# Performance work log

Hardware: AMD Instinct MI355X
Metric: run time of the kernel (lower is better)

## Reference

```python
import jax, jax.numpy as jnp
import numpy as np

B, S, F_IN, F_OUT = 8, 128, 768, 768
NUM_REL = 41           # num_dependencies + 1
NUM_LAYER = 2
N_HEAD, HID = 8, 96    # hidden_dim = embed_dim // n_head
EMB = 768


def setup_inputs() -> dict:
    key = jax.random.key(0)
    ks = jax.random.split(key, 14)
    s = 1.0 / np.sqrt(F_IN)
    inp = {
        "x": jax.random.normal(ks[0], (B, S, F_IN), dtype=jnp.float32),
        "adj": jax.random.uniform(ks[1], (B, NUM_REL, S, S), dtype=jnp.float32),
        "q": jax.random.normal(ks[2], (B, EMB), dtype=jnp.float32),
        # R-GCN params (stacked over layers)
        "w_rgcn": jax.random.uniform(ks[3], (NUM_LAYER, NUM_REL, F_IN, F_OUT), minval=-s, maxval=s),
        "score_w": jax.random.uniform(ks[4], (NUM_LAYER, F_OUT), minval=-s, maxval=s),
        "score_b": jax.random.uniform(ks[5], (NUM_LAYER,), minval=-s, maxval=s),
        # Attention params (stored as [in, out] for x @ W)
        "wk": jax.random.uniform(ks[6], (EMB, N_HEAD * HID), minval=-s, maxval=s),
        "bk": jnp.zeros((N_HEAD * HID,), jnp.float32),
        "wq": jax.random.uniform(ks[7], (EMB, N_HEAD * HID), minval=-s, maxval=s),
        "bq": jnp.zeros((N_HEAD * HID,), jnp.float32),
        "wbil": jax.random.uniform(ks[8], (HID, HID), minval=-1.0 / np.sqrt(HID), maxval=1.0 / np.sqrt(HID)),
        "wproj": jax.random.uniform(ks[9], (N_HEAD * HID, EMB), minval=-s, maxval=s),
        "bproj": jnp.zeros((EMB,), jnp.float32),
    }
    return inp


def _rgcn_layer(h, adj, w, sw, sb):
    # h: [B,S,I]; adj: [B,R,S,S]; w: [R,I,O]
    hidden = jnp.einsum("bsi,rio->brso", h, w)            # per-relation transform
    denom = jnp.sum(adj, axis=3, keepdims=True)           # [B,R,S,1]
    intm = jnp.einsum("brsk,brko->brso", adj, hidden)     # relation-wise aggregation
    div = intm / jnp.where(denom == 0, jnp.ones_like(denom), denom)
    logits = jnp.einsum("brso,o->brs", div, sw) + sb      # score Linear(out->1)
    r_coeffs = jax.nn.softmax(logits, axis=1)             # softmax over relations
    out = jnp.einsum("brso,brs->bso", div, r_coeffs)
    return jax.nn.relu(out)


def _attention(k, q, wk, bk, wq, bq, wbil, wproj, bproj):
    # k: [B,S,E]; q: [B,E] -> [B,1,E]
    q3 = q[:, None, :]
    kx = (k @ wk + bk).reshape(B, S, N_HEAD, HID)
    qx = (q3 @ wq + bq).reshape(B, 1, N_HEAD, HID)
    qw = jnp.einsum("bqhd,de->bqhe", qx, wbil)            # bi_linear score
    score = jnp.einsum("bqhe,bkhe->bhqk", qw, kx)
    attn = jax.nn.softmax(score, axis=-1)
    o = jnp.einsum("bhqk,bkhd->bqhd", attn, kx).reshape(B, 1, N_HEAD * HID)
    return o @ wproj + bproj                              # [B,1,EMB]


def reference(x, adj, q, w_rgcn, score_w, score_b, wk, bk, wq, bq, wbil, wproj, bproj):
    h = x
    for l in range(NUM_LAYER):
        h = _rgcn_layer(h, adj, w_rgcn[l], score_w[l], score_b[l])
    return _attention(h, q, wk, bk, wq, bq, wbil, wproj, bproj)
```

## Files before the change

kernel.cpp:

```cpp
#include <hip/hip_runtime.h>
#include <stdint.h>

#define B_ 8
#define S_ 128
#define R_ 41
#define F_ 768
#define NH_ 8
#define HID_ 96
#define BS_ (B_*S_)
#define SM_SCALE 256.0f
#define NG_ 21
#define NWV_ (R_*12)

typedef _Float16 f16;
typedef _Float16 f16x8 __attribute__((ext_vector_type(8)));
typedef _Float16 f16x4 __attribute__((ext_vector_type(4)));
typedef _Float16 f16x2 __attribute__((ext_vector_type(2)));
typedef float f32x4 __attribute__((ext_vector_type(4)));
typedef float f32x2 __attribute__((ext_vector_type(2)));

#define GLD16(gp, lp) __builtin_amdgcn_global_load_lds((const __attribute__((address_space(1))) uint32_t*)(gp), (__attribute__((address_space(3))) uint32_t*)(lp), 16, 0, 0)

__device__ __forceinline__ float wredsum(float v){
  #pragma unroll
  for (int o=32;o;o>>=1) v += __shfl_down(v,o,64);
  return v;
}

__global__ __launch_bounds__(256) void kPrep(const float* __restrict__ w_rgcn, const float* __restrict__ score_w,
                                             const float* __restrict__ wk, const float* __restrict__ x,
                                             const float* __restrict__ qin, const float* __restrict__ wq,
                                             const float* __restrict__ bq, const float* __restrict__ wbil,
                                             f16* __restrict__ wT0, f16* __restrict__ wT1,
                                             float* __restrict__ v0, float* __restrict__ v1,
                                             f16* __restrict__ wkT, f16* __restrict__ h16T,
                                             float* __restrict__ qwb) {
  __shared__ float sbuf[64*68];
  int bid = blockIdx.x;
  int tid = threadIdx.x;
  if (bid < 2*NWV_) {
    int l = (bid >= NWV_);
    int sub = bid - l*NWV_;
    const float* w = w_rgcn + (size_t)l*R_*F_*F_;
    const float* sw = score_w + l*F_;
    f16* wT = l ? wT1 : wT0;
    float* v = l ? v1 : v0;
    int it = sub % 12, r = sub / 12;
    int ri = tid >> 2, c = tid & 3;
    float vacc = 0.f;
    for (int ot = 0; ot < 12; ++ot) {
      const float* src = w + ((size_t)r*F_ + (it*64 + ri))*F_ + ot*64 + c*16;
      const float* swp = sw + ot*64 + c*16;
      __syncthreads();
      #pragma unroll
      for (int j=0;j<4;j++){
        f32x4 v4 = *(const f32x4*)(src + j*4);
        f32x4 s4 = *(const f32x4*)(swp + j*4);
        vacc += v4.x*s4.x + v4.y*s4.y + v4.z*s4.z + v4.w*s4.w;
        *(f32x4*)&sbuf[ri*68 + c*16 + j*4] = v4;
      }
      __syncthreads();
      int ro = tid >> 2;
      f16 outv[16];
      #pragma unroll
      for (int j=0;j<16;j++) outv[j] = (f16)sbuf[(c*16+j)*68 + ro];
      f16* dst = wT + ((size_t)r*F_ + (ot*64+ro))*F_ + it*64 + c*16;
      *(f16x8*)dst = *(f16x8*)&outv[0];
      *(f16x8*)(dst+8) = *(f16x8*)&outv[8];
    }
    vacc += __shfl_down(vacc, 1, 64);
    vacc += __shfl_down(vacc, 2, 64);
    if (c == 0) v[(size_t)r*F_ + it*64 + ri] = vacc;
  } else if (bid < 2*NWV_ + 144) {
    int sub = bid - 2*NWV_;
    int ot = sub % 12; int it = sub / 12;
    int ri = tid >> 2, c = tid & 3;
    const float* src = wk + (size_t)(it*64 + ri)*F_ + ot*64 + c*16;
    #pragma unroll
    for (int j=0;j<4;j++){
      f32x4 v4 = *(const f32x4*)(src + j*4);
      *(f32x4*)&sbuf[ri*68 + c*16 + j*4] = v4;
    }
    __syncthreads();
    int ro = tid >> 2;
    f16 outv[16];
    #pragma unroll
    for (int j=0;j<16;j++) outv[j] = (f16)sbuf[(c*16+j)*68 + ro];
    f16* dst = wkT + (size_t)(ot*64+ro)*F_ + it*64 + c*16;
    *(f16x8*)dst = *(f16x8*)&outv[0];
    *(f16x8*)(dst+8) = *(f16x8*)&outv[8];
  } else if (bid < 2*NWV_ + 144 + 192) {
    int sub = bid - (2*NWV_ + 144);
    int st = sub & 1; int ft = (sub>>1) % 12; int b = sub / 24;
    f16* t = (f16*)sbuf;
    int sl = tid>>2, c = tid&3;
    const float* src = x + ((size_t)b*S_ + st*64 + sl)*F_ + ft*64 + c*16;
    f16 tmp[16];
    #pragma unroll
    for (int j=0;j<16;j++) tmp[j] = (f16)src[j];
    *(f16x8*)&t[sl*72 + c*16]     = *(f16x8*)&tmp[0];
    *(f16x8*)&t[sl*72 + c*16 + 8] = *(f16x8*)&tmp[8];
    __syncthreads();
    int fl = tid>>2;
    f16 outv[16];
    #pragma unroll
    for (int j=0;j<16;j++) outv[j] = t[(c*16+j)*72 + fl];
    f16* dst = h16T + ((size_t)b*F_ + ft*64 + fl)*S_ + st*64 + c*16;
    *(f16x8*)dst = *(f16x8*)&outv[0];
    *(f16x8*)(dst+8) = *(f16x8*)&outv[8];
  } else {
    int sub = bid - (2*NWV_ + 144 + 192);
    int h = sub & 7, b = sub >> 3;
    float* q_s = sbuf;
    float* qx_s = sbuf + 768;
    for (int j=tid; j<F_; j+=256) q_s[j] = qin[(size_t)b*F_ + j];
    __syncthreads();
    if (tid < 192){
      int e = tid>>1, half = tid&1;
      const float* wp = wq + (size_t)(half*384)*F_ + h*HID_ + e;
      const float* qp = q_s + half*384;
      float a0=0.f,a1=0.f,a2=0.f,a3=0.f;
      for (int i=0;i<384;i+=4){
        a0 += qp[i]  *wp[(size_t)i*F_];
        a1 += qp[i+1]*wp[(size_t)(i+1)*F_];
        a2 += qp[i+2]*wp[(size_t)(i+2)*F_];
        a3 += qp[i+3]*wp[(size_t)(i+3)*F_];
      }
      float s2 = a0+a1+a2+a3;
      s2 += __shfl_xor(s2,1,64);
      if (half==0) qx_s[e] = s2 + bq[h*HID_+e];
    }
    __syncthreads();
    if (tid < HID_){
      float a0=0.f,a1=0.f,a2=0.f,a3=0.f;
      for (int d=0;d<HID_;d+=4){
        a0 += qx_s[d]  *wbil[(size_t)d*HID_+tid];
        a1 += qx_s[d+1]*wbil[(size_t)(d+1)*HID_+tid];
        a2 += qx_s[d+2]*wbil[(size_t)(d+2)*HID_+tid];
        a3 += qx_s[d+3]*wbil[(size_t)(d+3)*HID_+tid];
      }
      qwb[(size_t)b*F_ + h*HID_ + tid] = a0+a1+a2+a3;
    }
  }
}

__global__ __launch_bounds__(256) void kUL(const float* __restrict__ h, const float* __restrict__ v,
                    const float* __restrict__ adj, const float* __restrict__ sb_all, int l,
                    float* __restrict__ dinv, float* __restrict__ lg) {
  int bid = blockIdx.x;
  int r = bid % R_, b = bid / R_;
  __shared__ float v_s[F_];
  __shared__ float u_s[S_];
  int tid = threadIdx.x;
  #pragma unroll
  for (int j=0;j<3;j++) v_s[tid + j*256] = v[(size_t)r*F_ + tid + j*256];
  __syncthreads();
  int wid = tid>>6, lane = tid&63;
  for (int kl=0; kl<32; ++kl){
    int k = wid*32 + kl;
    const float* hr = h + ((size_t)b*S_ + k)*F_ + lane*12;
    const float* vp = &v_s[lane*12];
    float acc=0.f;
    #pragma unroll
    for (int j=0;j<3;j++){
      f32x4 a = *(const f32x4*)(hr+j*4);
      f32x4 c4 = *(const f32x4*)(vp+j*4);
      acc += a.x*c4.x+a.y*c4.y+a.z*c4.z+a.w*c4.w;
    }
    acc = wredsum(acc);
    if (lane==0) u_s[k] = acc;
  }
  __syncthreads();
  int s = tid>>1, half = tid&1;
  const float* arow = adj + ((size_t)bid*S_ + s)*S_ + half*64;
  const float* up = &u_s[half*64];
  float ssum=0.f, sdot=0.f;
  #pragma unroll
  for (int j=0;j<16;j++){
    f32x4 a = *(const f32x4*)(arow + j*4);
    ssum += a.x+a.y+a.z+a.w;
    sdot += a.x*up[j*4] + a.y*up[j*4+1] + a.z*up[j*4+2] + a.w*up[j*4+3];
  }
  ssum += __shfl_xor(ssum,1,64);
  sdot += __shfl_xor(sdot,1,64);
  if (half==0){
    float dv = (ssum==0.0f)?1.0f:(1.0f/ssum);
    dinv[(size_t)bid*S_ + s] = dv;
    lg[(size_t)bid*S_ + s] = sdot*dv + sb_all[l];
  }
}

__global__ __launch_bounds__(64) void kSM16(const float* __restrict__ lg, const float* __restrict__ dinv,
                     const float* __restrict__ adj, f16* __restrict__ M) {
  int bid = blockIdx.x;
  int b = bid >> 7, s = bid & 127;
  int lane = threadIdx.x;
  __shared__ float coef[R_];
  float x = (lane < R_) ? lg[((size_t)b*R_ + lane)*S_ + s] : -1e30f;
  float m = x;
  #pragma unroll
  for (int o=32;o;o>>=1) m = fmaxf(m, __shfl_xor(m,o,64));
  float e = (lane < R_) ? expf(x - m) : 0.f;
  float sum = e;
  #pragma unroll
  for (int o=32;o;o>>=1) sum += __shfl_xor(sum,o,64);
  if (lane < R_) coef[lane] = e/sum * SM_SCALE * dinv[((size_t)b*R_ + lane)*S_ + s];
  __syncthreads();
  for (int r=0;r<R_;r++){
    float cc = coef[r];
    size_t base = (((size_t)(b*R_+r))*S_ + s)*S_ + lane*2;
    f32x2 a2 = *(const f32x2*)(adj + base);
    f16x2 o2; o2[0]=(f16)(a2.x*cc); o2[1]=(f16)(a2.y*cc);
    *(f16x2*)(M + base) = o2;
  }
}

__global__ __launch_bounds__(256) void kGgemm(const f16* __restrict__ M, const f16* __restrict__ hT, f16* __restrict__ G) {
  __shared__ f16 lds[2*16384];
  f16* lsA = lds;
  f16* lsB = lds + 16384;
  int bid = blockIdx.x;
  int nt = bid % 6; int r = (bid/6) % R_; int b = bid/(6*R_);
  int tid = threadIdx.x, wid = tid>>6, lane = tid&63;
  const f16* Ab = M + (size_t)(b*R_ + r)*(S_*S_);
  const f16* Bb = hT + ((size_t)b*F_ + nt*128)*S_;
  #pragma unroll
  for (int j=0;j<8;j++){
    int qd = wid*8 + j;
    GLD16(Ab + qd*512 + lane*8, lsA + qd*512);
    GLD16(Bb + qd*512 + lane*8, lsB + qd*512);
  }
  __syncthreads();
  f32x4 acc[4][4] = {};
  int wr = wid>>1, wc = wid&1;
  int lr = lane&15, kk0 = (lane>>4)*8;
  #pragma unroll
  for (int ks=0;ks<4;ks++){
    int kk = ks*32 + kk0;
    f16x8 av[4], bv[4];
    #pragma unroll
    for (int i=0;i<4;i++) av[i] = *(const f16x8*)&lsA[(wr*64+i*16+lr)*128 + kk];
    #pragma unroll
    for (int i=0;i<4;i++) bv[i] = *(const f16x8*)&lsB[(wc*64+i*16+lr)*128 + kk];
    #pragma unroll
    for (int mi=0;mi<4;mi++)
      #pragma unroll
      for (int ni=0;ni<4;ni++)
        acc[mi][ni] = __builtin_amdgcn_mfma_f32_16x16x32_f16(av[mi],bv[ni],acc[mi][ni],0,0,0);
  }
  __syncthreads();
  #pragma unroll
  for (int mi=0;mi<4;mi++)
    #pragma unroll
    for (int ni=0;ni<4;ni++){
      int row = wr*64 + mi*16 + (lane>>4)*4;
      int col = wc*64 + ni*16 + lr;
      #pragma unroll
      for (int i=0;i<4;i++)
        lds[(row+i)*136 + col] = (f16)acc[mi][ni][i];
    }
  __syncthreads();
  int row = tid>>1, seg = tid&1;
  f16* dst = G + ((size_t)(b*R_ + r)*S_ + row)*F_ + nt*128 + seg*64;
  const f16* sl = lds + row*136 + seg*64;
  #pragma unroll
  for (int j=0;j<8;j++) *(f16x8*)(dst + j*8) = *(const f16x8*)(sl + j*8);
}

__global__ __launch_bounds__(512,2) void kOutGemm(const f16* __restrict__ G, const f16* __restrict__ WT, float* __restrict__ Cp) {
  __shared__ f16 ls[2][2][256*64];
  int bid = blockIdx.x;
  int t12 = bid % 12, g = bid / 12;
  int nt = t12 % 3, mt = t12 / 3;
  int r0 = (g<20)? 2*g : 40;
  int nr = (g<20)? 2 : 1;
  int tid = threadIdx.x, wid = tid>>6, lane = tid&63;
  size_t abase[4], bbase[4];
  #pragma unroll
  for (int j=0;j<4;j++){
    int chunk = wid*4 + j;
    int arow = mt*256 + chunk*8 + (lane>>3);
    int b = arow >> 7, s = arow & 127;
    abase[j] = ((size_t)b*R_*S_ + s)*(size_t)F_ + (lane&7)*8;
    int orow = nt*256 + chunk*8 + (lane>>3);
    bbase[j] = (size_t)orow*F_ + (lane&7)*8;
  }
  f32x4 acc[8][4] = {};
  int wr = wid>>2, wc = wid&3;
  int lr = lane&15, kk0 = (lane>>4)*8;
  int nsteps = nr*12;
  auto STAGE = [&](int bf, int step){
    int r = r0 + step/12, it = step%12;
    const f16* Ar = G  + (size_t)r*S_*F_;
    const f16* Br = WT + (size_t)r*F_*F_;
    #pragma unroll
    for (int j=0;j<4;j++){
      int chunk = wid*4 + j;
      GLD16(Ar + abase[j] + it*64, &ls[bf][0][chunk*512]);
      GLD16(Br + bbase[j] + it*64, &ls[bf][1][chunk*512]);
    }
  };
  STAGE(0, 0);
  __syncthreads();
  int cur = 0;
  for (int step=0; step<nsteps; ++step){
    if (step+1 < nsteps) STAGE(cur^1, step+1);
    __builtin_amdgcn_s_setprio(1);
    #pragma unroll
    for (int ks=0;ks<2;ks++){
      int kk = ks*32 + kk0;
      f16x8 av[8], bv[4];
      #pragma unroll
      for (int i=0;i<8;i++) av[i] = *(const f16x8*)&ls[cur][0][(wr*128+i*16+lr)*64 + kk];
      #pragma unroll
      for (int i=0;i<4;i++) bv[i] = *(const f16x8*)&ls[cur][1][(wc*64+i*16+lr)*64 + kk];
      #pragma unroll
      for (int mi=0;mi<8;mi++)
        #pragma unroll
        for (int ni=0;ni<4;ni++)
          acc[mi][ni] = __builtin_amdgcn_mfma_f32_16x16x32_f16(av[mi],bv[ni],acc[mi][ni],0,0,0);
    }
    __builtin_amdgcn_s_setprio(0);
    __syncthreads();
    cur ^= 1;
  }
  #pragma unroll
  for (int mi=0;mi<8;mi++)
    #pragma unroll
    for (int ni=0;ni<4;ni++){
      int row = mt*256 + wr*128 + mi*16 + (lane>>4)*4;
      int col = nt*256 + wc*64 + ni*16 + lr;
      #pragma unroll
      for (int i=0;i<4;i++)
        Cp[((size_t)g*BS_ + row + i)*F_ + col] = acc[mi][ni][i];
    }
}

__global__ __launch_bounds__(256) void kReduceT(const float* __restrict__ Cp, float* __restrict__ h32,
                                                f16* __restrict__ h16o, f16* __restrict__ hT) {
  int bid = blockIdx.x;
  int st = bid & 1; int ft = (bid>>1) % 12; int b = bid / 24;
  __shared__ f16 t[64*72];
  int tid = threadIdx.x;
  int sl = tid>>2, c = tid&3;
  size_t base = ((size_t)(b*S_ + st*64 + sl))*F_ + ft*64 + c*16;
  const float inv = 1.0f/SM_SCALE;
  f16 tmp[16];
  #pragma unroll
  for (int q=0;q<4;q++){
    f32x4 s4 = {};
    #pragma unroll
    for (int g=0; g<NG_; g++){
      f32x4 v4 = *(const f32x4*)(Cp + (size_t)g*BS_*F_ + base + q*4);
      s4.x += v4.x; s4.y += v4.y; s4.z += v4.z; s4.w += v4.w;
    }
    f32x4 rr;
    rr.x = fmaxf(s4.x*inv, 0.f); rr.y = fmaxf(s4.y*inv, 0.f);
    rr.z = fmaxf(s4.z*inv, 0.f); rr.w = fmaxf(s4.w*inv, 0.f);
    *(f32x4*)(h32 + base + q*4) = rr;
    tmp[q*4+0]=(f16)rr.x; tmp[q*4+1]=(f16)rr.y; tmp[q*4+2]=(f16)rr.z; tmp[q*4+3]=(f16)rr.w;
  }
  *(f16x8*)&t[sl*72 + c*16]     = *(f16x8*)&tmp[0];
  *(f16x8*)&t[sl*72 + c*16 + 8] = *(f16x8*)&tmp[8];
  *(f16x8*)(h16o + base)     = *(f16x8*)&tmp[0];
  *(f16x8*)(h16o + base + 8) = *(f16x8*)&tmp[8];
  __syncthreads();
  int fl = tid>>2;
  f16 outv[16];
  #pragma unroll
  for (int j=0;j<16;j++) outv[j] = t[(c*16+j)*72 + fl];
  f16* dst = hT + ((size_t)b*F_ + ft*64 + fl)*S_ + st*64 + c*16;
  *(f16x8*)dst = *(f16x8*)&outv[0];
  *(f16x8*)(dst+8) = *(f16x8*)&outv[8];
}

__global__ __launch_bounds__(256) void kKx(const f16* __restrict__ A, const f16* __restrict__ BT,
                    const float* __restrict__ bias, float* __restrict__ C) {
  __shared__ f16 ls[2][2][128*64];
  int bid = blockIdx.x;
  int nt = bid % 6, mt = bid / 6;
  int tid = threadIdx.x, wid = tid>>6, lane = tid&63;
  size_t abase[4], bbase[4];
  #pragma unroll
  for (int j=0;j<4;j++){
    int qd = wid*4 + j;
    int row = mt*128 + qd*8 + (lane>>3);
    abase[j] = (size_t)row*F_ + (lane&7)*8;
    int o = nt*128 + qd*8 + (lane>>3);
    bbase[j] = (size_t)o*F_ + (lane&7)*8;
  }
  f32x4 acc[4][4] = {};
  int wr = wid>>1, wc = wid&1;
  int lr = lane&15, kk0 = (lane>>4)*8;
  auto STAGE = [&](int bf, int it){
    #pragma unroll
    for (int j=0;j<4;j++){
      int qd = wid*4+j;
      GLD16(A + abase[j] + it*64, &ls[bf][0][qd*512]);
      GLD16(BT + bbase[j] + it*64, &ls[bf][1][qd*512]);
    }
  };
  STAGE(0, 0);
  __syncthreads();
  int cur = 0;
  for (int it=0; it<12; ++it){
    if (it+1 < 12) STAGE(cur^1, it+1);
    #pragma unroll
    for (int ks=0;ks<2;ks++){
      int kk = ks*32 + kk0;
      f16x8 av[4], bv[4];
      #pragma unroll
      for (int i=0;i<4;i++) av[i] = *(const f16x8*)&ls[cur][0][(wr*64+i*16+lr)*64 + kk];
      #pragma unroll
      for (int i=0;i<4;i++) bv[i] = *(const f16x8*)&ls[cur][1][(wc*64+i*16+lr)*64 + kk];
      #pragma unroll
      for (int mi=0;mi<4;mi++)
        #pragma unroll
        for (int ni=0;ni<4;ni++)
          acc[mi][ni] = __builtin_amdgcn_mfma_f32_16x16x32_f16(av[mi],bv[ni],acc[mi][ni],0,0,0);
    }
    __syncthreads();
    cur ^= 1;
  }
  #pragma unroll
  for (int mi=0;mi<4;mi++)
    #pragma unroll
    for (int ni=0;ni<4;ni++){
      int row = mt*128 + wr*64 + mi*16 + (lane>>4)*4;
      int col = nt*128 + wc*64 + ni*16 + lr;
      float bb = bias[col];
      #pragma unroll
      for (int i=0;i<4;i++)
        C[(size_t)(row+i)*F_ + col] = acc[mi][ni][i] + bb;
    }
}

__global__ __launch_bounds__(256) void kAttnCore(const float* __restrict__ kx, const float* __restrict__ qw,
                                                 float* __restrict__ obuf) {
  int bid = blockIdx.x; int h = bid & 7; int b = bid >> 3;
  __shared__ float qw_s[HID_], sc[S_];
  __shared__ float smax, ssum;
  int t = threadIdx.x;
  if (t < HID_) qw_s[t] = qw[(size_t)b*F_ + h*HID_ + t];
  __syncthreads();
  {
    int k = t>>1, half = t&1;
    const float* kp = kx + ((size_t)b*S_ + k)*F_ + h*HID_ + half*48;
    const float* qp = &qw_s[half*48];
    float a0=0.f,a1=0.f;
    #pragma unroll
    for (int e=0;e<48;e+=8){
      f32x4 k0 = *(const f32x4*)(kp+e);
      f32x4 k1 = *(const f32x4*)(kp+e+4);
      a0 += k0.x*qp[e]+k0.y*qp[e+1]+k0.z*qp[e+2]+k0.w*qp[e+3];
      a1 += k1.x*qp[e+4]+k1.y*qp[e+5]+k1.z*qp[e+6]+k1.w*qp[e+7];
    }
    float s2 = a0+a1;
    s2 += __shfl_xor(s2,1,64);
    if (half==0) sc[k] = s2;
  }
  __syncthreads();
  if (t < 64) {
    float m = fmaxf(sc[t], sc[t+64]);
    #pragma unroll
    for (int o=32;o;o>>=1) m = fmaxf(m, __shfl_down(m,o,64));
    if (t==0) smax = m;
  }
  __syncthreads();
  if (t < S_) sc[t] = expf(sc[t]-smax);
  __syncthreads();
  if (t < 64) {
    float s = sc[t] + sc[t+64];
    s = wredsum(s);
    if (t==0) ssum = s;
  }
  __syncthreads();
  if (t < 192) {
    int d = t>>1, kh = (t&1)*64;
    const float* kp = kx + ((size_t)b*S_ + kh)*F_ + h*HID_ + d;
    float a0=0.f,a1=0.f,a2=0.f,a3=0.f;
    #pragma unroll
    for (int k=0;k<64;k+=4){
      a0 += sc[kh+k]  *kp[(size_t)k*F_];
      a1 += sc[kh+k+1]*kp[(size_t)(k+1)*F_];
      a2 += sc[kh+k+2]*kp[(size_t)(k+2)*F_];
      a3 += sc[kh+k+3]*kp[(size_t)(k+3)*F_];
    }
    float s2 = a0+a1+a2+a3;
    s2 += __shfl_xor(s2,1,64);
    if ((t&1)==0) obuf[(size_t)b*F_ + h*HID_ + d] = s2/ssum;
  }
}

__global__ __launch_bounds__(256) void kProj(const float* __restrict__ obuf, const float* __restrict__ wproj,
                      const float* __restrict__ bproj, float* __restrict__ outp) {
  int bid = blockIdx.x; int b = bid/3, seg = bid%3;
  int t = threadIdx.x;
  __shared__ float ov[F_];
  for (int j=t;j<F_;j+=256) ov[j] = obuf[(size_t)b*F_ + j];
  __syncthreads();
  int col = seg*256 + t;
  float a0=0.f,a1=0.f,a2=0.f,a3=0.f;
  for (int j=0;j<F_;j+=4){
    a0 += ov[j]*wproj[(size_t)j*F_+col];
    a1 += ov[j+1]*wproj[(size_t)(j+1)*F_+col];
    a2 += ov[j+2]*wproj[(size_t)(j+2)*F_+col];
    a3 += ov[j+3]*wproj[(size_t)(j+3)*F_+col];
  }
  outp[(size_t)b*F_ + col] = bproj[col] + a0+a1+a2+a3;
}

extern "C" void kernel_launch(void* const* d_in, const int* in_sizes, int n_in,
                              void* d_out, int out_size, void* d_ws, size_t ws_size,
                              hipStream_t stream) {
  (void)in_sizes; (void)n_in; (void)out_size;
  const float* x      = (const float*)d_in[0];
  const float* adj    = (const float*)d_in[1];
  const float* qin    = (const float*)d_in[2];
  const float* w_rgcn = (const float*)d_in[3];
  const float* score_w= (const float*)d_in[4];
  const float* score_b= (const float*)d_in[5];
  const float* wk     = (const float*)d_in[6];
  const float* bk     = (const float*)d_in[7];
  const float* wq     = (const float*)d_in[8];
  const float* bq     = (const float*)d_in[9];
  const float* wbil   = (const float*)d_in[10];
  const float* wproj  = (const float*)d_in[11];
  const float* bproj  = (const float*)d_in[12];
  float* outp = (float*)d_out;

  char* p = (char*)d_ws;
  auto alloc = [&](size_t bytes)->char* {
    char* r = p; p += (bytes + 255) & ~(size_t)255; return r;
  };
  f16*   w16T0 = (f16*)  alloc((size_t)R_*F_*F_*2);
  f16*   w16T1 = (f16*)  alloc((size_t)R_*F_*F_*2);
  f16*   G16   = (f16*)  alloc((size_t)B_*R_*S_*F_*2);
  f16*   M16   = (f16*)  alloc((size_t)B_*R_*S_*S_*2);
  float* Cpart = (float*)alloc((size_t)NG_*BS_*F_*4);
  float* h32a  = (float*)alloc((size_t)BS_*F_*4);
  f16*   h16row= (f16*)  alloc((size_t)BS_*F_*2);
  f16*   h16T  = (f16*)  alloc((size_t)BS_*F_*2);
  float* kx    = (float*)alloc((size_t)BS_*F_*4);
  f16*   wkT   = (f16*)  alloc((size_t)F_*F_*2);
  float* vbuf0 = (float*)alloc((size_t)R_*F_*4);
  float* vbuf1 = (float*)alloc((size_t)R_*F_*4);
  float* dinv  = (float*)alloc((size_t)B_*R_*S_*4);
  float* lgb   = (float*)alloc((size_t)B_*R_*S_*4);
  float* qwb   = (float*)alloc((size_t)B_*F_*4);
  float* obuf  = (float*)alloc((size_t)B_*F_*4);
  if ((size_t)(p - (char*)d_ws) > ws_size) return;

  kPrep<<<2*NWV_ + 144 + 192 + 64, 256, 0, stream>>>(
      w_rgcn, score_w, wk, x, qin, wq, bq, wbil,
      w16T0, w16T1, vbuf0, vbuf1, wkT, h16T, qwb);

  kUL<<<B_*R_, 256, 0, stream>>>(x, vbuf0, adj, score_b, 0, dinv, lgb);
  kSM16<<<B_*S_, 64, 0, stream>>>(lgb, dinv, adj, M16);
  kGgemm<<<B_*R_*6, 256, 0, stream>>>(M16, h16T, G16);
  kOutGemm<<<12*NG_, 512, 0, stream>>>(G16, w16T0, Cpart);
  kReduceT<<<192, 256, 0, stream>>>(Cpart, h32a, h16row, h16T);

  kUL<<<B_*R_, 256, 0, stream>>>(h32a, vbuf1, adj, score_b, 1, dinv, lgb);
  kSM16<<<B_*S_, 64, 0, stream>>>(lgb, dinv, adj, M16);
  kGgemm<<<B_*R_*6, 256, 0, stream>>>(M16, h16T, G16);
  kOutGemm<<<12*NG_, 512, 0, stream>>>(G16, w16T1, Cpart);
  kReduceT<<<192, 256, 0, stream>>>(Cpart, h32a, h16row, h16T);

  kKx<<<48, 256, 0, stream>>>(h16row, wkT, bk, kx);
  kAttnCore<<<64, 256, 0, stream>>>(kx, qwb, obuf);
  kProj<<<24, 256, 0, stream>>>(obuf, wproj, bproj, outp);
}
```

Before: 483.0 us.

## Rebalance small kernels: coalesced q projection, per-thread kUL dots, 4-wave kSM16

```diff
diff --git a/kernel.cpp b/kernel.cpp
--- a/kernel.cpp
+++ b/kernel.cpp
@@ -30,11 +30,11 @@
 __global__ __launch_bounds__(256) void kPrep(const float* __restrict__ w_rgcn, const float* __restrict__ score_w,
                                              const float* __restrict__ wk, const float* __restrict__ x,
                                              const float* __restrict__ qin, const float* __restrict__ wq,
-                                             const float* __restrict__ bq, const float* __restrict__ wbil,
+                                             const float* __restrict__ bq,
                                              f16* __restrict__ wT0, f16* __restrict__ wT1,
                                              float* __restrict__ v0, float* __restrict__ v1,
                                              f16* __restrict__ wkT, f16* __restrict__ h16T,
-                                             float* __restrict__ qwb) {
+                                             float* __restrict__ qxb) {
   __shared__ float sbuf[64*68];
   int bid = blockIdx.x;
   int tid = threadIdx.x;
@@ -110,37 +110,19 @@
     *(f16x8*)(dst+8) = *(f16x8*)&outv[8];
   } else {
     int sub = bid - (2*NWV_ + 144 + 192);
-    int h = sub & 7, b = sub >> 3;
+    int b = sub/3, seg = sub%3;
     float* q_s = sbuf;
-    float* qx_s = sbuf + 768;
-    for (int j=tid; j<F_; j+=256) q_s[j] = qin[(size_t)b*F_ + j];
+    for (int j=tid;j<F_;j+=256) q_s[j] = qin[(size_t)b*F_ + j];
     __syncthreads();
-    if (tid < 192){
-      int e = tid>>1, half = tid&1;
-      const float* wp = wq + (size_t)(half*384)*F_ + h*HID_ + e;
-      const float* qp = q_s + half*384;
-      float a0=0.f,a1=0.f,a2=0.f,a3=0.f;
-      for (int i=0;i<384;i+=4){
-        a0 += qp[i]  *wp[(size_t)i*F_];
-        a1 += qp[i+1]*wp[(size_t)(i+1)*F_];
-        a2 += qp[i+2]*wp[(size_t)(i+2)*F_];
-        a3 += qp[i+3]*wp[(size_t)(i+3)*F_];
-      }
-      float s2 = a0+a1+a2+a3;
-      s2 += __shfl_xor(s2,1,64);
-      if (half==0) qx_s[e] = s2 + bq[h*HID_+e];
-    }
-    __syncthreads();
-    if (tid < HID_){
-      float a0=0.f,a1=0.f,a2=0.f,a3=0.f;
-      for (int d=0;d<HID_;d+=4){
-        a0 += qx_s[d]  *wbil[(size_t)d*HID_+tid];
-        a1 += qx_s[d+1]*wbil[(size_t)(d+1)*HID_+tid];
-        a2 += qx_s[d+2]*wbil[(size_t)(d+2)*HID_+tid];
-        a3 += qx_s[d+3]*wbil[(size_t)(d+3)*HID_+tid];
-      }
-      qwb[(size_t)b*F_ + h*HID_ + tid] = a0+a1+a2+a3;
-    }
+    int col = seg*256 + tid;
+    float a0=0.f,a1=0.f,a2=0.f,a3=0.f;
+    for (int i=0;i<F_;i+=4){
+      a0 += q_s[i]  *wq[(size_t)i*F_+col];
+      a1 += q_s[i+1]*wq[(size_t)(i+1)*F_+col];
+      a2 += q_s[i+2]*wq[(size_t)(i+2)*F_+col];
+      a3 += q_s[i+3]*wq[(size_t)(i+3)*F_+col];
+    }
+    qxb[(size_t)b*F_ + col] = bq[col] + a0+a1+a2+a3;
   }
 }
 
@@ -155,20 +137,25 @@
   #pragma unroll
   for (int j=0;j<3;j++) v_s[tid + j*256] = v[(size_t)r*F_ + tid + j*256];
   __syncthreads();
-  int wid = tid>>6, lane = tid&63;
-  for (int kl=0; kl<32; ++kl){
-    int k = wid*32 + kl;
-    const float* hr = h + ((size_t)b*S_ + k)*F_ + lane*12;
-    const float* vp = &v_s[lane*12];
-    float acc=0.f;
-    #pragma unroll
-    for (int j=0;j<3;j++){
-      f32x4 a = *(const f32x4*)(hr+j*4);
-      f32x4 c4 = *(const f32x4*)(vp+j*4);
-      acc += a.x*c4.x+a.y*c4.y+a.z*c4.z+a.w*c4.w;
-    }
-    acc = wredsum(acc);
-    if (lane==0) u_s[k] = acc;
+  {
+    int k = tid>>1, half = tid&1;
+    const float* hr = h + ((size_t)b*S_ + k)*F_ + half*384;
+    const float* vp = &v_s[half*384];
+    float a0=0.f,a1=0.f,a2=0.f,a3=0.f;
+    #pragma unroll 4
+    for (int j=0;j<384;j+=16){
+      f32x4 x0 = *(const f32x4*)(hr+j);    f32x4 y0 = *(const f32x4*)(vp+j);
+      f32x4 x1 = *(const f32x4*)(hr+j+4);  f32x4 y1 = *(const f32x4*)(vp+j+4);
+      f32x4 x2 = *(const f32x4*)(hr+j+8);  f32x4 y2 = *(const f32x4*)(vp+j+8);
+      f32x4 x3 = *(const f32x4*)(hr+j+12); f32x4 y3 = *(const f32x4*)(vp+j+12);
+      a0 += x0.x*y0.x+x0.y*y0.y+x0.z*y0.z+x0.w*y0.w;
+      a1 += x1.x*y1.x+x1.y*y1.y+x1.z*y1.z+x1.w*y1.w;
+      a2 += x2.x*y2.x+x2.y*y2.y+x2.z*y2.z+x2.w*y2.w;
+      a3 += x3.x*y3.x+x3.y*y3.y+x3.z*y3.z+x3.w*y3.w;
+    }
+    float s2 = (a0+a1)+(a2+a3);
+    s2 += __shfl_xor(s2,1,64);
+    if (half==0) u_s[k] = s2;
   }
   __syncthreads();
   int s = tid>>1, half = tid&1;
@@ -190,23 +177,25 @@
   }
 }
 
-__global__ __launch_bounds__(64) void kSM16(const float* __restrict__ lg, const float* __restrict__ dinv,
+__global__ __launch_bounds__(256) void kSM16(const float* __restrict__ lg, const float* __restrict__ dinv,
                      const float* __restrict__ adj, f16* __restrict__ M) {
   int bid = blockIdx.x;
   int b = bid >> 7, s = bid & 127;
-  int lane = threadIdx.x;
+  int tid = threadIdx.x, lane = tid&63, wid = tid>>6;
   __shared__ float coef[R_];
-  float x = (lane < R_) ? lg[((size_t)b*R_ + lane)*S_ + s] : -1e30f;
-  float m = x;
-  #pragma unroll
-  for (int o=32;o;o>>=1) m = fmaxf(m, __shfl_xor(m,o,64));
-  float e = (lane < R_) ? expf(x - m) : 0.f;
-  float sum = e;
-  #pragma unroll
-  for (int o=32;o;o>>=1) sum += __shfl_xor(sum,o,64);
-  if (lane < R_) coef[lane] = e/sum * SM_SCALE * dinv[((size_t)b*R_ + lane)*S_ + s];
-  __syncthreads();
-  for (int r=0;r<R_;r++){
+  if (wid==0){
+    float x = (lane < R_) ? lg[((size_t)b*R_ + lane)*S_ + s] : -1e30f;
+    float m = x;
+    #pragma unroll
+    for (int o=32;o;o>>=1) m = fmaxf(m, __shfl_xor(m,o,64));
+    float e = (lane < R_) ? expf(x - m) : 0.f;
+    float sum = e;
+    #pragma unroll
+    for (int o=32;o;o>>=1) sum += __shfl_xor(sum,o,64);
+    if (lane < R_) coef[lane] = e/sum * SM_SCALE * dinv[((size_t)b*R_ + lane)*S_ + s];
+  }
+  __syncthreads();
+  for (int r=wid; r<R_; r+=4){
     float cc = coef[r];
     size_t base = (((size_t)(b*R_+r))*S_ + s)*S_ + lane*2;
     f32x2 a2 = *(const f32x2*)(adj + base);
@@ -435,13 +424,24 @@
     }
 }
 
-__global__ __launch_bounds__(256) void kAttnCore(const float* __restrict__ kx, const float* __restrict__ qw,
-                                                 float* __restrict__ obuf) {
+__global__ __launch_bounds__(256) void kAttnCore(const float* __restrict__ kx, const float* __restrict__ qx,
+                                                 const float* __restrict__ wbil, float* __restrict__ obuf) {
   int bid = blockIdx.x; int h = bid & 7; int b = bid >> 3;
-  __shared__ float qw_s[HID_], sc[S_];
+  __shared__ float qx_s[HID_], qw_s[HID_], sc[S_];
   __shared__ float smax, ssum;
   int t = threadIdx.x;
-  if (t < HID_) qw_s[t] = qw[(size_t)b*F_ + h*HID_ + t];
+  if (t < HID_) qx_s[t] = qx[(size_t)b*F_ + h*HID_ + t];
+  __syncthreads();
+  if (t < HID_) {
+    float a0=0.f,a1=0.f,a2=0.f,a3=0.f;
+    for (int d=0;d<HID_;d+=4){
+      a0 += qx_s[d]  *wbil[(size_t)d*HID_+t];
+      a1 += qx_s[d+1]*wbil[(size_t)(d+1)*HID_+t];
+      a2 += qx_s[d+2]*wbil[(size_t)(d+2)*HID_+t];
+      a3 += qx_s[d+3]*wbil[(size_t)(d+3)*HID_+t];
+    }
+    qw_s[t] = a0+a1+a2+a3;
+  }
   __syncthreads();
   {
     int k = t>>1, half = t&1;
@@ -547,27 +547,27 @@
   float* vbuf1 = (float*)alloc((size_t)R_*F_*4);
   float* dinv  = (float*)alloc((size_t)B_*R_*S_*4);
   float* lgb   = (float*)alloc((size_t)B_*R_*S_*4);
-  float* qwb   = (float*)alloc((size_t)B_*F_*4);
+  float* qxb   = (float*)alloc((size_t)B_*F_*4);
   float* obuf  = (float*)alloc((size_t)B_*F_*4);
   if ((size_t)(p - (char*)d_ws) > ws_size) return;
 
-  kPrep<<<2*NWV_ + 144 + 192 + 64, 256, 0, stream>>>(
-      w_rgcn, score_w, wk, x, qin, wq, bq, wbil,
-      w16T0, w16T1, vbuf0, vbuf1, wkT, h16T, qwb);
+  kPrep<<<2*NWV_ + 144 + 192 + 24, 256, 0, stream>>>(
+      w_rgcn, score_w, wk, x, qin, wq, bq,
+      w16T0, w16T1, vbuf0, vbuf1, wkT, h16T, qxb);
 
   kUL<<<B_*R_, 256, 0, stream>>>(x, vbuf0, adj, score_b, 0, dinv, lgb);
-  kSM16<<<B_*S_, 64, 0, stream>>>(lgb, dinv, adj, M16);
+  kSM16<<<B_*S_, 256, 0, stream>>>(lgb, dinv, adj, M16);
   kGgemm<<<B_*R_*6, 256, 0, stream>>>(M16, h16T, G16);
   kOutGemm<<<12*NG_, 512, 0, stream>>>(G16, w16T0, Cpart);
   kReduceT<<<192, 256, 0, stream>>>(Cpart, h32a, h16row, h16T);
 
   kUL<<<B_*R_, 256, 0, stream>>>(h32a, vbuf1, adj, score_b, 1, dinv, lgb);
-  kSM16<<<B_*S_, 64, 0, stream>>>(lgb, dinv, adj, M16);
+  kSM16<<<B_*S_, 256, 0, stream>>>(lgb, dinv, adj, M16);
   kGgemm<<<B_*R_*6, 256, 0, stream>>>(M16, h16T, G16);
   kOutGemm<<<12*NG_, 512, 0, stream>>>(G16, w16T1, Cpart);
   kReduceT<<<192, 256, 0, stream>>>(Cpart, h32a, h16row, h16T);
 
   kKx<<<48, 256, 0, stream>>>(h16row, wkT, bk, kx);
-  kAttnCore<<<64, 256, 0, stream>>>(kx, qwb, obuf);
+  kAttnCore<<<64, 256, 0, stream>>>(kx, qxb, wbil, obuf);
   kProj<<<24, 256, 0, stream>>>(obuf, wproj, bproj, outp);
 }
```

Result: slower. 504.1 us (+4.4%).
